# Kernel tuning notes

Measured on AMD Instinct MI355X. Metric: run time of the kernel, lower is better.

Reference implementation:

```python
import jax, jax.numpy as jnp
import numpy as np

F = 256  # filters
FQ = F // 8  # query/key channels


def setup_inputs() -> dict:
    key = jax.random.key(0)
    ks = jax.random.split(key, 9)
    B, H, W = 4, 64, 64
    s_in = 1.0 / np.sqrt(F)
    inp = {
        "inputs": jax.random.normal(ks[0], (B, H, W, F), jnp.float32),
        "Wq": jax.random.normal(ks[1], (F, FQ), jnp.float32) * s_in,
        "bq": jnp.zeros((FQ,), jnp.float32),
        "Wk": jax.random.normal(ks[2], (F, FQ), jnp.float32) * s_in,
        "bk": jnp.zeros((FQ,), jnp.float32),
        "Wv": jax.random.normal(ks[3], (F, F), jnp.float32) * s_in,
        "bv": jnp.zeros((F,), jnp.float32),
        "Wo": jax.random.normal(ks[4], (F, F), jnp.float32) * s_in,
        "bo": jnp.zeros((F,), jnp.float32),
    }
    return inp


def reference(inputs, Wq, bq, Wk, bk, Wv, bv, Wo, bo):
    B, H, W, C = inputs.shape
    N = H * W
    x = inputs.reshape(B, N, C)  # 1x1 conv == per-token linear
    q = jax.nn.relu(jnp.einsum('bnc,cd->bnd', x, Wq) + bq)  # [B,N,FQ]
    k = jax.nn.relu(jnp.einsum('bnc,cd->bnd', x, Wk) + bk)  # [B,N,FQ]
    v = jax.nn.relu(jnp.einsum('bnc,cd->bnd', x, Wv) + bv)  # [B,N,C]
    # unscaled full attention (as in the original module)
    attn = jax.nn.softmax(jnp.einsum('bnd,bmd->bnm', q, k), axis=-1)  # [B,N,N]
    attended = jnp.einsum('bnm,bmc->bnc', attn, v)  # [B,N,C]
    out = jax.nn.relu(jnp.einsum('bnc,cd->bnd', attended, Wo) + bo)
    return inputs + out.reshape(B, H, W, C)
```

## Files before the change

### kernel.cpp

```cpp
#include <hip/hip_runtime.h>

typedef __attribute__((ext_vector_type(8))) short short8;
typedef __attribute__((ext_vector_type(4))) float floatx4;

#define MFMA16(a, b, c) __builtin_amdgcn_mfma_f32_16x16x32_bf16((a), (b), (c), 0, 0, 0)

#define LDP 72
#define LDO 264
#define LOG2E 1.4426950408889634f
#define PSHIFT 23.083120654223414f

__device__ __forceinline__ float bf2f(unsigned short u) {
  return __uint_as_float(((unsigned int)u) << 16);
}
__device__ __forceinline__ unsigned short f2bf(float f) {
  unsigned int x = __float_as_uint(f);
  x += 0x7FFFu + ((x >> 16) & 1u);
  return (unsigned short)(x >> 16);
}
__device__ __forceinline__ float ld_in(const void* p, long i, int isf32) {
  if (isf32) return ((const float*)p)[i];
  return bf2f(((const unsigned short*)p)[i]);
}
__device__ __forceinline__ short8 ld16(const unsigned short* p) {
  return *(const short8*)__builtin_assume_aligned(p, 16);
}
__device__ __forceinline__ void st16(unsigned short* p, short8 v) {
  *(short8*)__builtin_assume_aligned(p, 16) = v;
}
__device__ __forceinline__ int detect_bad(const unsigned short* x, int idx) {
  const short8 v = ld16(x + (long)idx * 8);
  int bad = 0;
#pragma unroll
  for (int j = 0; j < 8; j++) {
    const unsigned int e = (((unsigned short)v[j]) >> 7) & 0xFFu;
    if (e >= 141u) bad = 1;
  }
  return bad;
}


__global__ __launch_bounds__(256)
void proj_kernel(const void* __restrict__ x,
                 const void* __restrict__ Wq, const void* __restrict__ bq,
                 const void* __restrict__ Wk, const void* __restrict__ bk,
                 const void* __restrict__ Wv, const void* __restrict__ bv,
                 const void* __restrict__ Wo,
                 unsigned short* __restrict__ Qf, unsigned short* __restrict__ Kf,
                 unsigned short* __restrict__ Vf, unsigned short* __restrict__ Wf_o) {
  __shared__ unsigned short Wl[64][LDO];
  __shared__ unsigned short Vl[64][LDP];
  __shared__ int flagl[4];
  const int t = (int)threadIdx.x;
  const int wave = t >> 6, lane = t & 63, quad = lane >> 4, l15 = lane & 15;

  {
    const int bad = detect_bad((const unsigned short*)x, t) |
                    detect_bad((const unsigned short*)x, 256 + t);
    if (lane == 0) flagl[wave] = (__ballot(bad) != 0ull) ? 1 : 0;
  }
  __syncthreads();
  const int isf32 = flagl[0] | flagl[1] | flagl[2] | flagl[3];

  const int blk = (int)blockIdx.x;
  if (blk >= 1280) {
    const int b2 = blk - 1280;
    const int g0 = (b2 >> 2) * 64, c0 = (b2 & 3) * 64;
    const int j = t & 63, r4 = t >> 6;
#pragma unroll
    for (int k2 = 0; k2 < 16; k2++) {
      const int rr = r4 * 16 + k2;
      Vl[j][rr] = f2bf(ld_in(Wo, (long)(c0 + rr) * 256 + g0 + j, isf32));
    }
    __syncthreads();
#pragma unroll
    for (int cc = 0; cc < 2; cc++) {
      const int c = t + cc * 256;
      const int f_l = c >> 6, lane_c = c & 63;
      const int og = f_l >> 1, kse = f_l & 1;
      const int out_l = lane_c & 15, q = lane_c >> 4;
      const short8 v = ld16(&Vl[og * 16 + out_l][kse * 32 + q * 8]);
      st16(Wf_o + (long)(((g0 >> 4) + og) * 8 + (c0 >> 5) + kse) * 512 + lane_c * 8, v);
    }
    return;
  }

  const int ct = blk % 5;
  const long row_base = (long)(blk / 5) * 64;

  if (ct == 0) {
    for (int i = t; i < 16384; i += 256) {
      const int g = i & 63, c = i >> 6;
      const float v = (g < 32) ? ld_in(Wq, (long)c * 32 + g, isf32) * LOG2E
                               : ld_in(Wk, (long)c * 32 + (g - 32), isf32);
      Wl[g][c] = f2bf(v);
    }
  } else {
    const int g0 = (ct - 1) * 64;
    for (int i = t; i < 16384; i += 256) {
      const int j = i & 63, c = i >> 6;
      Wl[j][c] = f2bf(ld_in(Wv, (long)c * 256 + g0 + j, isf32));
    }
  }
  __syncthreads();

  const long arow = row_base + wave * 16 + l15;
  floatx4 acc[4];
  acc[0] = acc[1] = acc[2] = acc[3] = (floatx4)0.0f;

#pragma unroll
  for (int ks = 0; ks < 8; ks++) {
    short8 a;
    if (isf32) {
      const float* xf = (const float*)x + arow * 256 + ks * 32 + quad * 8;
      floatx4 f0 = *(const floatx4*)xf;
      floatx4 f1 = *(const floatx4*)(xf + 4);
#pragma unroll
      for (int j = 0; j < 4; j++) { a[j] = (short)f2bf(f0[j]); a[4 + j] = (short)f2bf(f1[j]); }
    } else {
      a = ld16((const unsigned short*)x + arow * 256 + ks * 32 + quad * 8);
    }
#pragma unroll
    for (int tn = 0; tn < 4; tn++) {
      const short8 bfr = ld16(&Wl[tn * 16 + l15][ks * 32 + quad * 8]);
      acc[tn] = MFMA16(a, bfr, acc[tn]);
    }
  }

  if (ct == 0) {
#pragma unroll
    for (int tn = 0; tn < 4; tn++) {
      const int g = tn * 16 + l15;
      const float bias = (g < 32) ? ld_in(bq, g, isf32) * LOG2E
                                  : ld_in(bk, g - 32, isf32);
#pragma unroll
      for (int r = 0; r < 4; r++)
        Vl[wave * 16 + quad * 4 + r][g] = f2bf(fmaxf(acc[tn][r] + bias, 0.0f));
    }
    __syncthreads();
    const long f0 = row_base >> 4;
#pragma unroll
    for (int cc = 0; cc < 2; cc++) {
      const int c = t + cc * 256;
      const int isK = c >> 8;
      const int c2 = c & 255;
      const int f_l = c2 >> 6, lane_c = c2 & 63;
      const int row_l = lane_c & 15, q = lane_c >> 4;
      const short8 v = ld16(&Vl[f_l * 16 + row_l][isK * 32 + q * 8]);
      unsigned short* dst = isK ? Kf : Qf;
      st16(dst + (f0 + f_l) * 512 + lane_c * 8, v);
    }
  } else {
#pragma unroll
    for (int tn = 0; tn < 4; tn++) {
      const float bias = ld_in(bv, (long)(ct - 1) * 64 + tn * 16 + l15, isf32);
#pragma unroll
      for (int r = 0; r < 4; r++)
        Vl[tn * 16 + l15][wave * 16 + quad * 4 + r] =
            f2bf(fmaxf(acc[tn][r] + bias, 0.0f));
    }
    __syncthreads();
    const long bb = row_base >> 12;
    const int kt = (int)((row_base & 4095) >> 6);
    const long fbase = (bb * 64 + kt) * 32 + (long)(ct - 1) * 8;
#pragma unroll
    for (int cc = 0; cc < 2; cc++) {
      const int c = t * 2 + cc;
      const int f_l = c >> 6, lane_c = c & 63;
      const int cg = f_l >> 1, kh = f_l & 1;
      const int ch_l = lane_c & 15, q = lane_c >> 4;
      const short8 v = ld16(&Vl[cg * 16 + ch_l][kh * 32 + q * 8]);
      st16(Vf + (fbase + f_l) * 512 + lane_c * 8, v);
    }
  }
}

__global__ __launch_bounds__(512, 2)
void flash_kernel(const unsigned short* __restrict__ Qf,
                  const unsigned short* __restrict__ Kf,
                  const unsigned short* __restrict__ Vf,
                  const unsigned short* __restrict__ Wf_o,
                  const void* __restrict__ bo,
                  const void* __restrict__ xin, void* __restrict__ out) {
  __shared__ unsigned short Pl[2][64 * LDP];
  __shared__ unsigned short Ol[64 * LDO];
  __shared__ float Lp[2][64];
  __shared__ float Ll[64];
  __shared__ int flagl[8];

  const int t = (int)threadIdx.x;
  const int wave = t >> 6, lane = t & 63, quad = lane >> 4, l15 = lane & 15;

  {
    const int bad = detect_bad((const unsigned short*)xin, t);
    if (lane == 0) flagl[wave] = (__ballot(bad) != 0ull) ? 1 : 0;
  }

  const int raw = (int)blockIdx.x;
  const int b = raw & 3;
  const int mt = raw >> 2;
  const long qrow0 = (long)b * 4096 + (long)mt * 64;
  const int m = wave & 3, h = wave >> 2;

  const long kfrag0 = (long)b * 256;
  const long vfrag0 = (long)b * 64 * 32;

  const short8 qf = ld16(Qf + ((qrow0 >> 4) + m) * 512 + lane * 8);
  short8 kb[2];
#pragma unroll
  for (int i = 0; i < 2; i++)
    kb[i] = ld16(Kf + (kfrag0 + h * 2 + i) * 512 + lane * 8);

  floatx4 oacc[4][2];
#pragma unroll
  for (int i = 0; i < 4; i++) { oacc[i][0] = (floatx4)0.0f; oacc[i][1] = (floatx4)0.0f; }
  float lpart[4] = {0.0f, 0.0f, 0.0f, 0.0f};

  for (int kt = 0; kt < 64; kt++) {
    short8 vb[2][2];
#pragma unroll
    for (int tv = 0; tv < 2; tv++)
#pragma unroll
      for (int kh = 0; kh < 2; kh++)
        vb[tv][kh] = ld16(Vf + (vfrag0 + (long)kt * 32 + (wave * 2 + tv) * 2 + kh) * 512 + lane * 8);

    floatx4 s[2];
#pragma unroll
    for (int i = 0; i < 2; i++) { s[i] = (floatx4)0.0f; s[i] = MFMA16(qf, kb[i], s[i]); }
    const int ktn = (kt + 1) & 63;
#pragma unroll
    for (int i = 0; i < 2; i++)
      kb[i] = ld16(Kf + (kfrag0 + ktn * 4 + h * 2 + i) * 512 + lane * 8);

    unsigned short* pl = Pl[kt & 1];
#pragma unroll
    for (int i = 0; i < 2; i++)
#pragma unroll
      for (int r = 0; r < 4; r++) {
        const float p = exp2f(s[i][r] - PSHIFT);
        lpart[r] += p;
        pl[(m * 16 + quad * 4 + r) * LDP + h * 32 + i * 16 + l15] = f2bf(p);
      }
    __syncthreads();

    const unsigned short* plr = Pl[kt & 1];
    short8 pa[4][2];
#pragma unroll
    for (int rm = 0; rm < 4; rm++)
#pragma unroll
      for (int kh = 0; kh < 2; kh++)
        pa[rm][kh] = ld16(&plr[(rm * 16 + l15) * LDP + kh * 32 + quad * 8]);

#pragma unroll
    for (int kh = 0; kh < 2; kh++)
#pragma unroll
      for (int tv = 0; tv < 2; tv++)
#pragma unroll
        for (int rm = 0; rm < 4; rm++)
          oacc[rm][tv] = MFMA16(pa[rm][kh], vb[tv][kh], oacc[rm][tv]);
  }

#pragma unroll
  for (int r = 0; r < 4; r++)
#pragma unroll
    for (int off = 1; off < 16; off <<= 1)
      lpart[r] += __shfl_xor(lpart[r], off);
  if (l15 == 0) {
    floatx4 lw;
#pragma unroll
    for (int r = 0; r < 4; r++) lw[r] = lpart[r];
    *(floatx4*)&Lp[h][m * 16 + quad * 4] = lw;
  }
  __syncthreads();
  if (t < 64) Ll[t] = 1.0f / (Lp[0][t] + Lp[1][t]);
  __syncthreads();

#pragma unroll
  for (int rm = 0; rm < 4; rm++) {
    const floatx4 ll = *(const floatx4*)&Ll[rm * 16 + quad * 4];
#pragma unroll
    for (int tv = 0; tv < 2; tv++)
#pragma unroll
      for (int r = 0; r < 4; r++)
        Ol[(rm * 16 + quad * 4 + r) * LDO + wave * 32 + tv * 16 + l15] =
            f2bf(oacc[rm][tv][r] * ll[r]);
  }
  __syncthreads();

  const int isf32 = flagl[0] | flagl[1] | flagl[2] | flagl[3] |
                    flagl[4] | flagl[5] | flagl[6] | flagl[7];
  const int m2 = wave & 3, gh = wave >> 2;
  floatx4 acc2[8];
#pragma unroll
  for (int i = 0; i < 8; i++) acc2[i] = (floatx4)0.0f;
#pragma unroll
  for (int ks = 0; ks < 8; ks++) {
    const short8 a = ld16(&Ol[(m2 * 16 + l15) * LDO + ks * 32 + quad * 8]);
#pragma unroll
    for (int tn = 0; tn < 8; tn++) {
      const short8 bfr = ld16(Wf_o + (long)((gh * 8 + tn) * 8 + ks) * 512 + lane * 8);
      acc2[tn] = MFMA16(a, bfr, acc2[tn]);
    }
  }
  __syncthreads();
#pragma unroll
  for (int tn = 0; tn < 8; tn++) {
    const int g = gh * 128 + tn * 16 + l15;
    const float bias = ld_in(bo, g, isf32);
#pragma unroll
    for (int r = 0; r < 4; r++)
      Ol[(m2 * 16 + quad * 4 + r) * LDO + g] = f2bf(fmaxf(acc2[tn][r] + bias, 0.0f));
  }
  __syncthreads();

  if (isf32) {
    const float* xf = (const float*)xin + qrow0 * 256;
    float* of = (float*)out + qrow0 * 256;
#pragma unroll
    for (int p = 0; p < 8; p++) {
      const int idx = p * 2048 + t * 4;
      const int row = idx >> 8, ch = idx & 255;
      floatx4 xv = *(const floatx4*)(xf + idx);
      floatx4 ov;
#pragma unroll
      for (int j = 0; j < 4; j++) ov[j] = bf2f(Ol[row * LDO + ch + j]) + xv[j];
      *(floatx4*)(of + idx) = ov;
    }
  } else {
    const unsigned short* xh = (const unsigned short*)xin + qrow0 * 256;
    unsigned short* oh = (unsigned short*)out + qrow0 * 256;
#pragma unroll
    for (int p = 0; p < 4; p++) {
      const int idx = p * 4096 + t * 8;
      const int row = idx >> 8, ch = idx & 255;
      const short8 xv = ld16(xh + idx);
      short8 ov;
#pragma unroll
      for (int j = 0; j < 8; j++)
        ov[j] = (short)f2bf(bf2f(Ol[row * LDO + ch + j]) + bf2f((unsigned short)xv[j]));
      st16(oh + idx, ov);
    }
  }
}

extern "C" void kernel_launch(void* const* d_in, const int* in_sizes, int n_in,
                              void* d_out, int out_size, void* d_ws, size_t ws_size,
                              hipStream_t stream) {
  const void* x  = d_in[0];
  const void* Wq = d_in[1]; const void* bq = d_in[2];
  const void* Wk = d_in[3]; const void* bk = d_in[4];
  const void* Wv = d_in[5]; const void* bv = d_in[6];
  const void* Wo = d_in[7]; const void* bo = d_in[8];

  char* ws = (char*)d_ws;
  unsigned short* Qf   = (unsigned short*)ws;
  unsigned short* Kf   = Qf + (long)4 * 4096 * 32;
  unsigned short* Vf   = Kf + (long)4 * 4096 * 32;
  unsigned short* Wf_o = Vf + (long)4 * 256 * 4096;

  proj_kernel<<<1296, 256, 0, stream>>>(x, Wq, bq, Wk, bk, Wv, bv, Wo,
                                        Qf, Kf, Vf, Wf_o);
  flash_kernel<<<256, 512, 0, stream>>>(Qf, Kf, Vf, Wf_o, bo, x, d_out);
}
```

Before: 202.1 us.

## Prepack weights once and software-pipeline QK softmax ahead of PV MFMAs

Adds a small prep kernel that converts and pre-swizzles the Wq/Wk/Wv/Wo weights into MFMA fragment layout once. The projection blocks can then read B fragments straight from global memory instead of each block rebuilding a 64x256 weight tile in LDS. The flash kernel is restructured so the QK^T score MFMA and exp for tile kt+1 run while the PV MFMAs for tile kt are issued, with one barrier per iteration, a K-tile prefetch two steps ahead and setprio around the PV MFMAs. It also swaps the operands of the QK MFMA so each lane holds one row sum, and uses packed v_cvt_pk_bf16 conversions with 8-byte LDS stores. The costs are an extra kernel launch and a different rounding path for the bf16 conversion.

```diff
diff --git a/kernel.cpp b/kernel.cpp
--- a/kernel.cpp
+++ b/kernel.cpp
@@ -2,6 +2,8 @@
 
 typedef __attribute__((ext_vector_type(8))) short short8;
 typedef __attribute__((ext_vector_type(4))) float floatx4;
+typedef __attribute__((ext_vector_type(2))) unsigned int uintx2;
+typedef __attribute__((ext_vector_type(4))) unsigned int uintx4;
 
 #define MFMA16(a, b, c) __builtin_amdgcn_mfma_f32_16x16x32_bf16((a), (b), (c), 0, 0, 0)
 
@@ -18,6 +20,11 @@
   x += 0x7FFFu + ((x >> 16) & 1u);
   return (unsigned short)(x >> 16);
 }
+__device__ __forceinline__ unsigned int cvt_pk_bf16(float lo, float hi) {
+  unsigned int r;
+  asm("v_cvt_pk_bf16_f32 %0, %1, %2" : "=v"(r) : "v"(lo), "v"(hi));
+  return r;
+}
 __device__ __forceinline__ float ld_in(const void* p, long i, int isf32) {
   if (isf32) return ((const float*)p)[i];
   return bf2f(((const unsigned short*)p)[i]);
@@ -41,19 +48,16 @@
 
 
 __global__ __launch_bounds__(256)
-void proj_kernel(const void* __restrict__ x,
-                 const void* __restrict__ Wq, const void* __restrict__ bq,
-                 const void* __restrict__ Wk, const void* __restrict__ bk,
-                 const void* __restrict__ Wv, const void* __restrict__ bv,
-                 const void* __restrict__ Wo,
-                 unsigned short* __restrict__ Qf, unsigned short* __restrict__ Kf,
-                 unsigned short* __restrict__ Vf, unsigned short* __restrict__ Wf_o) {
-  __shared__ unsigned short Wl[64][LDO];
+void prep_kernel(const void* __restrict__ x,
+                 const void* __restrict__ Wq, const void* __restrict__ Wk,
+                 const void* __restrict__ Wv, const void* __restrict__ Wo,
+                 unsigned short* __restrict__ Wf_qk,
+                 unsigned short* __restrict__ Wf_v,
+                 unsigned short* __restrict__ Wf_o) {
   __shared__ unsigned short Vl[64][LDP];
   __shared__ int flagl[4];
   const int t = (int)threadIdx.x;
-  const int wave = t >> 6, lane = t & 63, quad = lane >> 4, l15 = lane & 15;
-
+  const int wave = t >> 6, lane = t & 63;
   {
     const int bad = detect_bad((const unsigned short*)x, t) |
                     detect_bad((const unsigned short*)x, 256 + t);
@@ -63,14 +67,17 @@
   const int isf32 = flagl[0] | flagl[1] | flagl[2] | flagl[3];
 
   const int blk = (int)blockIdx.x;
-  if (blk >= 1280) {
-    const int b2 = blk - 1280;
+  const int j = t & 63, r4 = t >> 6;
+
+  if (blk < 32) {
+    const void* W = (blk < 16) ? Wo : Wv;
+    unsigned short* dst = (blk < 16) ? Wf_o : Wf_v;
+    const int b2 = blk & 15;
     const int g0 = (b2 >> 2) * 64, c0 = (b2 & 3) * 64;
-    const int j = t & 63, r4 = t >> 6;
 #pragma unroll
     for (int k2 = 0; k2 < 16; k2++) {
       const int rr = r4 * 16 + k2;
-      Vl[j][rr] = f2bf(ld_in(Wo, (long)(c0 + rr) * 256 + g0 + j, isf32));
+      Vl[j][rr] = f2bf(ld_in(W, (long)(c0 + rr) * 256 + g0 + j, isf32));
     }
     __syncthreads();
 #pragma unroll
@@ -80,31 +87,59 @@
       const int og = f_l >> 1, kse = f_l & 1;
       const int out_l = lane_c & 15, q = lane_c >> 4;
       const short8 v = ld16(&Vl[og * 16 + out_l][kse * 32 + q * 8]);
-      st16(Wf_o + (long)(((g0 >> 4) + og) * 8 + (c0 >> 5) + kse) * 512 + lane_c * 8, v);
-    }
-    return;
-  }
-
+      st16(dst + (long)(((g0 >> 4) + og) * 8 + (c0 >> 5) + kse) * 512 + lane_c * 8, v);
+    }
+  } else {
+    const int c0 = (blk - 32) * 64;
+#pragma unroll
+    for (int k2 = 0; k2 < 16; k2++) {
+      const int cl = r4 * 16 + k2;
+      const float v = (j < 32) ? ld_in(Wq, (long)(c0 + cl) * 32 + j, isf32) * LOG2E
+                               : ld_in(Wk, (long)(c0 + cl) * 32 + (j - 32), isf32);
+      Vl[j][cl] = f2bf(v);
+    }
+    __syncthreads();
+#pragma unroll
+    for (int cc = 0; cc < 2; cc++) {
+      const int c = t + cc * 256;
+      const int f_l = c >> 6, lane_c = c & 63;
+      const int og = f_l >> 1, kse = f_l & 1;
+      const int out_l = lane_c & 15, q = lane_c >> 4;
+      const short8 v = ld16(&Vl[og * 16 + out_l][kse * 32 + q * 8]);
+      st16(Wf_qk + (long)(og * 8 + (c0 >> 5) + kse) * 512 + lane_c * 8, v);
+    }
+  }
+}
+
+__global__ __launch_bounds__(256)
+void proj_kernel(const void* __restrict__ x,
+                 const void* __restrict__ bq, const void* __restrict__ bk,
+                 const void* __restrict__ bv,
+                 const unsigned short* __restrict__ Wf_qk,
+                 const unsigned short* __restrict__ Wf_v,
+                 unsigned short* __restrict__ Qf, unsigned short* __restrict__ Kf,
+                 unsigned short* __restrict__ Vf) {
+  __shared__ unsigned short Vl[64][LDP];
+  __shared__ int flagl[4];
+  const int t = (int)threadIdx.x;
+  const int wave = t >> 6, lane = t & 63, quad = lane >> 4, l15 = lane & 15;
+
+  {
+    const int bad = detect_bad((const unsigned short*)x, t) |
+                    detect_bad((const unsigned short*)x, 256 + t);
+    if (lane == 0) flagl[wave] = (__ballot(bad) != 0ull) ? 1 : 0;
+  }
+  __syncthreads();
+  const int isf32 = flagl[0] | flagl[1] | flagl[2] | flagl[3];
+
+  const int blk = (int)blockIdx.x;
   const int ct = blk % 5;
   const long row_base = (long)(blk / 5) * 64;
-
-  if (ct == 0) {
-    for (int i = t; i < 16384; i += 256) {
-      const int g = i & 63, c = i >> 6;
-      const float v = (g < 32) ? ld_in(Wq, (long)c * 32 + g, isf32) * LOG2E
-                               : ld_in(Wk, (long)c * 32 + (g - 32), isf32);
-      Wl[g][c] = f2bf(v);
-    }
-  } else {
-    const int g0 = (ct - 1) * 64;
-    for (int i = t; i < 16384; i += 256) {
-      const int j = i & 63, c = i >> 6;
-      Wl[j][c] = f2bf(ld_in(Wv, (long)c * 256 + g0 + j, isf32));
-    }
-  }
-  __syncthreads();
-
   const long arow = row_base + wave * 16 + l15;
+
+  const unsigned short* wb = (ct == 0) ? Wf_qk
+                                       : (Wf_v + (long)(ct - 1) * 4 * 8 * 512);
+
   floatx4 acc[4];
   acc[0] = acc[1] = acc[2] = acc[3] = (floatx4)0.0f;
 
@@ -113,16 +148,18 @@
     short8 a;
     if (isf32) {
       const float* xf = (const float*)x + arow * 256 + ks * 32 + quad * 8;
-      floatx4 f0 = *(const floatx4*)xf;
-      floatx4 f1 = *(const floatx4*)(xf + 4);
-#pragma unroll
-      for (int j = 0; j < 4; j++) { a[j] = (short)f2bf(f0[j]); a[4 + j] = (short)f2bf(f1[j]); }
+      const floatx4 f0 = *(const floatx4*)xf;
+      const floatx4 f1 = *(const floatx4*)(xf + 4);
+      uintx4 u;
+      u[0] = cvt_pk_bf16(f0[0], f0[1]); u[1] = cvt_pk_bf16(f0[2], f0[3]);
+      u[2] = cvt_pk_bf16(f1[0], f1[1]); u[3] = cvt_pk_bf16(f1[2], f1[3]);
+      a = *(short8*)&u;
     } else {
       a = ld16((const unsigned short*)x + arow * 256 + ks * 32 + quad * 8);
     }
 #pragma unroll
     for (int tn = 0; tn < 4; tn++) {
-      const short8 bfr = ld16(&Wl[tn * 16 + l15][ks * 32 + quad * 8]);
+      const short8 bfr = ld16(wb + (long)(tn * 8 + ks) * 512 + lane * 8);
       acc[tn] = MFMA16(a, bfr, acc[tn]);
     }
   }
@@ -206,15 +243,39 @@
   const long vfrag0 = (long)b * 64 * 32;
 
   const short8 qf = ld16(Qf + ((qrow0 >> 4) + m) * 512 + lane * 8);
+
+  floatx4 oacc[4][2];
+#pragma unroll
+  for (int i = 0; i < 4; i++) { oacc[i][0] = (floatx4)0.0f; oacc[i][1] = (floatx4)0.0f; }
+  float lpart = 0.0f;
+
   short8 kb[2];
 #pragma unroll
   for (int i = 0; i < 2; i++)
     kb[i] = ld16(Kf + (kfrag0 + h * 2 + i) * 512 + lane * 8);
-
-  floatx4 oacc[4][2];
-#pragma unroll
-  for (int i = 0; i < 4; i++) { oacc[i][0] = (floatx4)0.0f; oacc[i][1] = (floatx4)0.0f; }
-  float lpart[4] = {0.0f, 0.0f, 0.0f, 0.0f};
+  {
+    floatx4 s[2];
+#pragma unroll
+    for (int i = 0; i < 2; i++) { s[i] = (floatx4)0.0f; s[i] = MFMA16(kb[i], qf, s[i]); }
+    unsigned short* pl = Pl[0];
+#pragma unroll
+    for (int i = 0; i < 2; i++) {
+      const float p0 = exp2f(s[i][0] - PSHIFT);
+      const float p1 = exp2f(s[i][1] - PSHIFT);
+      const float p2 = exp2f(s[i][2] - PSHIFT);
+      const float p3 = exp2f(s[i][3] - PSHIFT);
+      lpart += (p0 + p1) + (p2 + p3);
+      uintx2 w;
+      w[0] = cvt_pk_bf16(p0, p1);
+      w[1] = cvt_pk_bf16(p2, p3);
+      *(uintx2*)__builtin_assume_aligned(
+          &pl[(m * 16 + l15) * LDP + h * 32 + i * 16 + quad * 4], 8) = w;
+    }
+  }
+#pragma unroll
+  for (int i = 0; i < 2; i++)
+    kb[i] = ld16(Kf + (kfrag0 + 4 + h * 2 + i) * 512 + lane * 8);
+  __syncthreads();
 
   for (int kt = 0; kt < 64; kt++) {
     short8 vb[2][2];
@@ -224,25 +285,6 @@
       for (int kh = 0; kh < 2; kh++)
         vb[tv][kh] = ld16(Vf + (vfrag0 + (long)kt * 32 + (wave * 2 + tv) * 2 + kh) * 512 + lane * 8);
 
-    floatx4 s[2];
-#pragma unroll
-    for (int i = 0; i < 2; i++) { s[i] = (floatx4)0.0f; s[i] = MFMA16(qf, kb[i], s[i]); }
-    const int ktn = (kt + 1) & 63;
-#pragma unroll
-    for (int i = 0; i < 2; i++)
-      kb[i] = ld16(Kf + (kfrag0 + ktn * 4 + h * 2 + i) * 512 + lane * 8);
-
-    unsigned short* pl = Pl[kt & 1];
-#pragma unroll
-    for (int i = 0; i < 2; i++)
-#pragma unroll
-      for (int r = 0; r < 4; r++) {
-        const float p = exp2f(s[i][r] - PSHIFT);
-        lpart[r] += p;
-        pl[(m * 16 + quad * 4 + r) * LDP + h * 32 + i * 16 + l15] = f2bf(p);
-      }
-    __syncthreads();
-
     const unsigned short* plr = Pl[kt & 1];
     short8 pa[4][2];
 #pragma unroll
@@ -251,6 +293,34 @@
       for (int kh = 0; kh < 2; kh++)
         pa[rm][kh] = ld16(&plr[(rm * 16 + l15) * LDP + kh * 32 + quad * 8]);
 
+    short8 kbn[2];
+    const int kt2 = (kt + 2) & 63;
+#pragma unroll
+    for (int i = 0; i < 2; i++)
+      kbn[i] = ld16(Kf + (kfrag0 + kt2 * 4 + h * 2 + i) * 512 + lane * 8);
+
+    if (kt < 63) {
+      floatx4 s[2];
+#pragma unroll
+      for (int i = 0; i < 2; i++) { s[i] = (floatx4)0.0f; s[i] = MFMA16(kb[i], qf, s[i]); }
+      unsigned short* pl = Pl[(kt + 1) & 1];
+#pragma unroll
+      for (int i = 0; i < 2; i++) {
+        const float p0 = exp2f(s[i][0] - PSHIFT);
+        const float p1 = exp2f(s[i][1] - PSHIFT);
+        const float p2 = exp2f(s[i][2] - PSHIFT);
+        const float p3 = exp2f(s[i][3] - PSHIFT);
+        lpart += (p0 + p1) + (p2 + p3);
+        uintx2 w;
+        w[0] = cvt_pk_bf16(p0, p1);
+        w[1] = cvt_pk_bf16(p2, p3);
+        *(uintx2*)__builtin_assume_aligned(
+            &pl[(m * 16 + l15) * LDP + h * 32 + i * 16 + quad * 4], 8) = w;
+      }
+    }
+    kb[0] = kbn[0]; kb[1] = kbn[1];
+
+    __builtin_amdgcn_s_setprio(1);
 #pragma unroll
     for (int kh = 0; kh < 2; kh++)
 #pragma unroll
@@ -258,19 +328,13 @@
 #pragma unroll
         for (int rm = 0; rm < 4; rm++)
           oacc[rm][tv] = MFMA16(pa[rm][kh], vb[tv][kh], oacc[rm][tv]);
-  }
-
-#pragma unroll
-  for (int r = 0; r < 4; r++)
-#pragma unroll
-    for (int off = 1; off < 16; off <<= 1)
-      lpart[r] += __shfl_xor(lpart[r], off);
-  if (l15 == 0) {
-    floatx4 lw;
-#pragma unroll
-    for (int r = 0; r < 4; r++) lw[r] = lpart[r];
-    *(floatx4*)&Lp[h][m * 16 + quad * 4] = lw;
-  }
+    __builtin_amdgcn_s_setprio(0);
+    __syncthreads();
+  }
+
+  lpart += __shfl_xor(lpart, 16);
+  lpart += __shfl_xor(lpart, 32);
+  if (lane < 16) Lp[h][m * 16 + lane] = lpart;
   __syncthreads();
   if (t < 64) Ll[t] = 1.0f / (Lp[0][t] + Lp[1][t]);
   __syncthreads();
@@ -353,12 +417,14 @@
   const void* Wo = d_in[7]; const void* bo = d_in[8];
 
   char* ws = (char*)d_ws;
-  unsigned short* Qf   = (unsigned short*)ws;
-  unsigned short* Kf   = Qf + (long)4 * 4096 * 32;
-  unsigned short* Vf   = Kf + (long)4 * 4096 * 32;
-  unsigned short* Wf_o = Vf + (long)4 * 256 * 4096;
-
-  proj_kernel<<<1296, 256, 0, stream>>>(x, Wq, bq, Wk, bk, Wv, bv, Wo,
-                                        Qf, Kf, Vf, Wf_o);
+  unsigned short* Qf    = (unsigned short*)ws;
+  unsigned short* Kf    = Qf + (long)4 * 4096 * 32;
+  unsigned short* Vf    = Kf + (long)4 * 4096 * 32;
+  unsigned short* Wf_o  = Vf + (long)4 * 256 * 4096;
+  unsigned short* Wf_v  = Wf_o + (long)128 * 512;
+  unsigned short* Wf_qk = Wf_v + (long)128 * 512;
+
+  prep_kernel<<<36, 256, 0, stream>>>(x, Wq, Wk, Wv, Wo, Wf_qk, Wf_v, Wf_o);
+  proj_kernel<<<1280, 256, 0, stream>>>(x, bq, bk, bv, Wf_qk, Wf_v, Qf, Kf, Vf);
   flash_kernel<<<256, 512, 0, stream>>>(Qf, Kf, Vf, Wf_o, bo, x, d_out);
 }
```

New measurement: 166.5 us. 1.21x faster.
